# Kernel tuning notes

Hardware: AMD Instinct MI355X
Metric: run time of the kernel (lower is better)

Reference implementation:

```python
import jax, jax.numpy as jnp
import numpy as np

WS = 8          # window size
HEADS = 16      # num heads

def conv2d(x, w, padding=0, groups=1):
    return jax.lax.conv_general_dilated(
        x, w, window_strides=(1, 1),
        padding=((padding, padding), (padding, padding)),
        feature_group_count=groups,
        dimension_numbers=('NCHW', 'OIHW', 'NCHW'))

def bn(x, scale, bias):  # inference BN folded into per-channel affine
    return x * scale[None, :, None, None] + bias[None, :, None, None]

def relative_position_index(ws):
    coords = np.stack(np.meshgrid(np.arange(ws), np.arange(ws), indexing='ij'))  # (2, ws, ws)
    cf = coords.reshape(2, -1)
    rc = (cf[:, :, None] - cf[:, None, :]).transpose(1, 2, 0)  # (n, n, 2)
    rc[:, :, 0] += ws - 1
    rc[:, :, 1] += ws - 1
    rc[:, :, 0] *= 2 * ws - 1
    return rc.sum(-1)  # (n, n) int

def avg_pool(x, kh, kw, ph, pw):
    # AvgPool2d with count_include_pad=True (zero pad, divide by full kernel size)
    s = jax.lax.reduce_window(x, 0.0, jax.lax.add, (1, 1, kh, kw), (1, 1, 1, 1),
                              ((0, 0), (0, 0), (ph, ph), (pw, pw)))
    return s / (kh * kw)

def setup_inputs() -> dict:
    key = jax.random.key(0)
    ks = jax.random.split(key, 12)
    C = 256
    x = jax.random.normal(ks[0], (4, C, 128, 128), dtype=jnp.float32)
    inp = {
        'x': x,
        'qkv_w':     jax.random.normal(ks[1], (3 * C, C, 1, 1), jnp.float32) * 0.05,
        'local1_w':  jax.random.normal(ks[2], (C, C, 3, 3), jnp.float32) * 0.05,
        'local1_scale': jnp.ones((C,), jnp.float32),
        'local1_bias':  jnp.zeros((C,), jnp.float32),
        'local2_w':  jax.random.normal(ks[3], (C, C, 1, 1), jnp.float32) * 0.05,
        'local2_scale': jnp.ones((C,), jnp.float32),
        'local2_bias':  jnp.zeros((C,), jnp.float32),
        'dw_w':      jax.random.normal(ks[4], (C, 1, WS, WS), jnp.float32) * 0.05,
        'proj_scale': jnp.ones((C,), jnp.float32),
        'proj_bias':  jnp.zeros((C,), jnp.float32),
        'pw_w':      jax.random.normal(ks[5], (C, C, 1, 1), jnp.float32) * 0.05,
        'rel_bias_table': jax.random.normal(ks[6], ((2 * WS - 1) ** 2, HEADS), jnp.float32) * 0.02,
    }
    return inp

def reference(x, qkv_w, local1_w, local1_scale, local1_bias,
              local2_w, local2_scale, local2_bias,
              dw_w, proj_scale, proj_bias, pw_w, rel_bias_table):
    B, C, H, W = x.shape
    ws, h = WS, HEADS
    d = C // h
    scale = d ** -0.5

    # local branches
    local = bn(conv2d(x, local2_w, padding=0), local2_scale, local2_bias) \
          + bn(conv2d(x, local1_w, padding=1), local1_scale, local1_bias)

    # reflect-pad to multiple of ws (static shapes)
    pad_h = (ws - H % ws) % ws
    pad_w = (ws - W % ws) % ws
    xp = x
    if pad_w:
        xp = jnp.pad(xp, ((0, 0), (0, 0), (0, 0), (0, pad_w)), mode='reflect')
    if pad_h:
        xp = jnp.pad(xp, ((0, 0), (0, 0), (0, pad_h), (0, 0)), mode='reflect')
    Hp, Wp = xp.shape[2], xp.shape[3]
    hh, ww = Hp // ws, Wp // ws

    # qkv: 1x1 conv, then window partition
    qkv = conv2d(xp, qkv_w)  # (B, 3C, Hp, Wp)
    qkv = qkv.reshape(B, 3, h, d, hh, ws, ww, ws)
    qkv = qkv.transpose(1, 0, 4, 6, 2, 5, 7, 3)  # (3, B, hh, ww, h, ws, ws, d)
    qkv = qkv.reshape(3, B * hh * ww, h, ws * ws, d)
    q, k, v = qkv[0], qkv[1], qkv[2]

    dots = jnp.einsum('whid,whjd->whij', q, k) * scale
    rpi = relative_position_index(ws)  # (n, n)
    bias = rel_bias_table[rpi.reshape(-1)].reshape(ws * ws, ws * ws, h)
    dots = dots + bias.transpose(2, 0, 1)[None]
    attn = jax.nn.softmax(dots, axis=-1)
    out = jnp.einsum('whij,whjd->whid', attn, v)

    # windows back to image
    out = out.reshape(B, hh, ww, h, ws, ws, d)
    out = out.transpose(0, 3, 6, 1, 4, 2, 5).reshape(B, C, Hp, Wp)
    out = out[:, :, :H, :W]

    # boundary smoothing avg pools (reflect pad 1 then zero-padded avg pool)
    ax = avg_pool(jnp.pad(out, ((0, 0), (0, 0), (0, 1), (0, 0)), mode='reflect'),
                  ws, 1, ws // 2 - 1, 0)
    ay = avg_pool(jnp.pad(out, ((0, 0), (0, 0), (0, 0), (0, 1)), mode='reflect'),
                  1, ws, 0, ws // 2 - 1)
    out = ax + ay + local

    # pad_out + separable conv projection
    out = jnp.pad(out, ((0, 0), (0, 0), (0, 1), (0, 1)), mode='reflect')
    out = conv2d(out, dw_w, padding=(ws - 1) // 2, groups=C)  # depthwise 8x8
    out = bn(out, proj_scale, proj_bias)
    out = conv2d(out, pw_w)  # pointwise 1x1
    return out[:, :, :H, :W]
```

## Files before the change

kernel.cpp:

```cpp
#include <hip/hip_runtime.h>
#include <cstddef>

#define HH 128
#define WW2 128
#define HWSZ (HH*WW2)
#define CCH 256

typedef __attribute__((ext_vector_type(8))) short short8v;
typedef __attribute__((ext_vector_type(16))) float f32x16;
typedef __attribute__((ext_vector_type(4)))  float f32x4;

__device__ __forceinline__ ushort bf16rte(float v) {
    uint u = __float_as_uint(v);
    uint r = u + 0x7FFFu + ((u >> 16) & 1u);
    return (ushort)(r >> 16);
}

__global__ __launch_bounds__(256) void k_fold(const float* __restrict__ l1w, const float* __restrict__ l1s,
                                              const float* __restrict__ l1b, const float* __restrict__ l2w,
                                              const float* __restrict__ l2s, const float* __restrict__ l2b,
                                              float* __restrict__ Wf, float* __restrict__ biasf) {
    int idx = blockIdx.x * 256 + threadIdx.x;
    if (idx < 2304 * 256) {
        int co = idx & 255;
        int i2 = idx >> 8;
        int ci = i2 / 9;
        int k  = i2 - ci * 9;
        float w = l1s[co] * l1w[co * 2304 + ci * 9 + k];
        if (k == 4) w += l2s[co] * l2w[co * 256 + ci];
        Wf[i2 * 256 + co] = w;
    }
    if (idx < 256) biasf[idx] = l1b[idx] + l2b[idx];
}

__global__ __launch_bounds__(256) void k_wsplit(const float* __restrict__ Wf,
                                                ushort* __restrict__ ahi, ushort* __restrict__ alo) {
    int idx = blockIdx.x * 256 + threadIdx.x;
    if (idx >= 589824) return;
    int j    = idx & 7;
    int lane = (idx >> 3) & 63;
    int t2   = idx >> 9;
    int kb   = t2 % 144;
    int cob  = t2 / 144;
    int cc  = kb / 18; int rem = kb - cc * 18; int tap = rem >> 1; int ks = rem & 1;
    int ci  = cc * 32 + ks * 16 + ((lane >> 5) << 3) + j;
    int co  = cob * 32 + (lane & 31);
    float v = Wf[(size_t)(ci * 9 + tap) * 256 + co];
    ushort h = bf16rte(v);
    float hf = __uint_as_float((uint)h << 16);
    ushort l = bf16rte(v - hf);
    ahi[idx] = h;
    alo[idx] = l;
}

__global__ __launch_bounds__(256) void k_aswz(const float* __restrict__ qkvw,
                                              ushort* __restrict__ aqh, ushort* __restrict__ aql) {
    int idx = blockIdx.x * 256 + threadIdx.x;
    if (idx >= 196608) return;
    int j    = idx & 7;
    int lane = (idx >> 3) & 63;
    int t2   = idx >> 9;
    int kk   = t2 & 7;
    int hp   = t2 >> 3;
    int p    = hp % 3, h = hp / 3;
    int co = p * 256 + h * 16 + (lane & 15);
    int ci = kk * 32 + ((lane >> 4) << 3) + j;
    float v = qkvw[(size_t)co * 256 + ci];
    ushort hi = bf16rte(v);
    float hf = __uint_as_float((uint)hi << 16);
    aqh[idx] = hi;
    aql[idx] = bf16rte(v - hf);
}

__global__ __launch_bounds__(256) void k_cvt(const float* __restrict__ x,
                                             ushort* __restrict__ xhi, ushort* __restrict__ xlo) {
    __shared__ uint pk[32 * 265];
    int t = threadIdx.x;
    int bid = blockIdx.x;
    int b = bid >> 9;
    int px0 = (bid & 511) * 32;
    const float* xb = x + (size_t)b * CCH * HWSZ;
    for (int step = 0; step < 32; ++step) {
        int ci = step * 8 + (t >> 5);
        float v = xb[(size_t)ci * HWSZ + px0 + (t & 31)];
        ushort h = bf16rte(v);
        float hf = __uint_as_float((uint)h << 16);
        ushort l = bf16rte(v - hf);
        pk[(t & 31) * 265 + ci] = ((uint)h << 16) | l;
    }
    __syncthreads();
    int pxl = t >> 3, o = t & 7;
    uint* hp = (uint*)xhi;
    uint* lp = (uint*)xlo;
    size_t pb2 = ((size_t)b * HWSZ + px0 + pxl) * 128;
#pragma unroll
    for (int m = 0; m < 16; ++m) {
        int cip = m * 16 + o * 2;
        uint p0 = pk[pxl * 265 + cip];
        uint p1 = pk[pxl * 265 + cip + 1];
        hp[pb2 + m * 8 + o] = (p1 & 0xFFFF0000u) | (p0 >> 16);
        lp[pb2 + m * 8 + o] = (p1 << 16) | (p0 & 0xFFFFu);
    }
}

__global__ __launch_bounds__(256) void k_conv3m(const ushort* __restrict__ xhi, const ushort* __restrict__ xlo,
                                                const ushort* __restrict__ afr_hi, const ushort* __restrict__ afr_lo,
                                                const float* __restrict__ biasf, float* __restrict__ outp) {
    __shared__ __align__(16) ushort Xsh[12960];
    char* xsb = (char*)Xsh;

    int t = threadIdx.x;
    int bid = blockIdx.x;
    int cb = bid & 1;
    int t2 = bid >> 1;
    int tile_c = t2 & 7;
    int tile_r = (t2 >> 3) & 15;
    int b = t2 >> 7;
    int x0 = tile_c * 16, y0 = tile_r * 8;

    int w = t >> 6, lane = t & 63;
    int co_w = cb * 128 + (w >> 1) * 64;
    int pr0 = (w & 1) * 4;
    int pr_l = (lane & 31) >> 4;
    int pc = lane & 15;
    int kl = lane >> 5;
    int lb0 = (pr0 + 0 + pr_l) * 1296 + pc * 72 + kl * 16;
    int lb1 = (pr0 + 2 + pr_l) * 1296 + pc * 72 + kl * 16;

    const short8v* Ahi = (const short8v*)afr_hi;
    const short8v* Alo = (const short8v*)afr_lo;
    int cobase = (co_w >> 5) * 144 * 64;

    f32x16 c00 = {}, c01 = {}, c10 = {}, c11 = {};

    for (int cc = 0; cc < 8; ++cc) {
        __syncthreads();
#pragma unroll
        for (int it = 0; it < 6; ++it) {
            int i = t + it * 256;
            if (i < 1440) {
                int oct = i & 3;
                int j2 = i >> 2;
                int plane = j2 & 1;
                int loc = j2 >> 1;
                int r = loc / 18, c = loc - r * 18;
                int gy = y0 - 1 + r, gx = x0 - 1 + c;
                uint4 v = make_uint4(0u, 0u, 0u, 0u);
                if (gy >= 0 && gy < 128 && gx >= 0 && gx < 128) {
                    const ushort* src = plane ? xlo : xhi;
                    v = *(const uint4*)(src + ((size_t)(b * HWSZ + gy * 128 + gx) * 256 + cc * 32 + oct * 8));
                }
                *(uint4*)(xsb + plane * 12960 + loc * 72 + oct * 16) = v;
            }
        }
        __syncthreads();

        int baseA = cobase + cc * 18 * 64 + lane;
#pragma unroll
        for (int tap = 0; tap < 9; ++tap) {
            const int ky = tap / 3, kx = tap - ky * 3;
#pragma unroll
            for (int ks = 0; ks < 2; ++ks) {
                const int boff = ky * 1296 + kx * 72 + ks * 32;
                short8v b0h = *(const short8v*)(xsb + lb0 + boff);
                short8v b0l = *(const short8v*)(xsb + lb0 + boff + 12960);
                short8v b1h = *(const short8v*)(xsb + lb1 + boff);
                short8v b1l = *(const short8v*)(xsb + lb1 + boff + 12960);
                int ai = baseA + (tap * 2 + ks) * 64;
                short8v a0h = Ahi[ai];
                short8v a0l = Alo[ai];
                short8v a1h = Ahi[ai + 144 * 64];
                short8v a1l = Alo[ai + 144 * 64];
                c00 = __builtin_amdgcn_mfma_f32_32x32x16_bf16(a0h, b0h, c00, 0, 0, 0);
                c00 = __builtin_amdgcn_mfma_f32_32x32x16_bf16(a0h, b0l, c00, 0, 0, 0);
                c00 = __builtin_amdgcn_mfma_f32_32x32x16_bf16(a0l, b0h, c00, 0, 0, 0);
                c01 = __builtin_amdgcn_mfma_f32_32x32x16_bf16(a0h, b1h, c01, 0, 0, 0);
                c01 = __builtin_amdgcn_mfma_f32_32x32x16_bf16(a0h, b1l, c01, 0, 0, 0);
                c01 = __builtin_amdgcn_mfma_f32_32x32x16_bf16(a0l, b1h, c01, 0, 0, 0);
                c10 = __builtin_amdgcn_mfma_f32_32x32x16_bf16(a1h, b0h, c10, 0, 0, 0);
                c10 = __builtin_amdgcn_mfma_f32_32x32x16_bf16(a1h, b0l, c10, 0, 0, 0);
                c10 = __builtin_amdgcn_mfma_f32_32x32x16_bf16(a1l, b0h, c10, 0, 0, 0);
                c11 = __builtin_amdgcn_mfma_f32_32x32x16_bf16(a1h, b1h, c11, 0, 0, 0);
                c11 = __builtin_amdgcn_mfma_f32_32x32x16_bf16(a1h, b1l, c11, 0, 0, 0);
                c11 = __builtin_amdgcn_mfma_f32_32x32x16_bf16(a1l, b1h, c11, 0, 0, 0);
            }
        }
    }

    int colg = x0 + pc;
    int row0 = y0 + pr0 + pr_l;
    int row1 = row0 + 2;
#pragma unroll
    for (int r = 0; r < 16; ++r) {
        int rr = (r & 3) + 8 * (r >> 2) + 4 * kl;
        {
            int co = co_w + rr;
            float bv = biasf[co];
            float* ob = outp + ((size_t)(b * CCH + co)) * HWSZ;
            ob[row0 * 128 + colg] = c00[r] + bv;
            ob[row1 * 128 + colg] = c01[r] + bv;
        }
        {
            int co = co_w + 32 + rr;
            float bv = biasf[co];
            float* ob = outp + ((size_t)(b * CCH + co)) * HWSZ;
            ob[row0 * 128 + colg] = c10[r] + bv;
            ob[row1 * 128 + colg] = c11[r] + bv;
        }
    }
}

__global__ __launch_bounds__(256) void k_attn(const ushort* __restrict__ xhi, const ushort* __restrict__ xlo,
                                              const ushort* __restrict__ aqh, const ushort* __restrict__ aql,
                                              const float* __restrict__ bt, float* __restrict__ attnout) {
    extern __shared__ float smem[];
    ushort* Bs  = (ushort*)smem;
    float* qkvb = smem + 16384;

    int t = threadIdx.x;
    int wv = __builtin_amdgcn_readfirstlane(t >> 6);
    int lane = t & 63;
    int widx = blockIdx.x;
    int b = widx >> 8;
    int rem = widx & 255;
    int hy = rem >> 4, wx = rem & 15;
    int y0 = hy * 8, x0 = wx * 8;

#pragma unroll
    for (int it = 0; it < 16; ++it) {
        int i = it * 256 + t;
        int plane = i >> 11;
        int r2 = i & 2047;
        int tok = r2 >> 5, ci8 = r2 & 31;
        int pix = (y0 + (tok >> 3)) * 128 + (x0 + (tok & 7));
        const ushort* src = plane ? xlo : xhi;
        uint4 v = *(const uint4*)(src + ((size_t)b * HWSZ + pix) * 256 + ci8 * 8);
        int lane2 = ((ci8 & 3) << 4) | (tok & 15);
        int fragid = (plane * 4 + (tok >> 4)) * 8 + (ci8 >> 2);
        *(uint4*)(Bs + (size_t)(fragid * 64 + lane2) * 8) = v;
    }
    __syncthreads();

    int irow = wv * 16 + (lane & 15);
    int jg = lane >> 4;
    int iy = irow >> 3, ix = irow & 7;
    int g0 = wv * 3;

    for (int h = 0; h < 16; ++h) {
        f32x4 c0 = {}, c1 = {}, c2 = {};
#pragma unroll
        for (int g = 0; g < 3; ++g) {
            int gid = g0 + g;
            int p = gid >> 2, tt = gid & 3;
            const short8v* Ah = (const short8v*)aqh + (size_t)((h * 3 + p) * 8) * 64 + lane;
            const short8v* Al = (const short8v*)aql + (size_t)((h * 3 + p) * 8) * 64 + lane;
            const short8v* Bh = (const short8v*)Bs + (tt * 8) * 64 + lane;
            const short8v* Bl = (const short8v*)Bs + ((4 + tt) * 8) * 64 + lane;
            f32x4 c = {};
#pragma unroll
            for (int kk = 0; kk < 8; ++kk) {
                short8v ah = Ah[kk * 64], al = Al[kk * 64];
                short8v bh = Bh[kk * 64], bl = Bl[kk * 64];
                c = __builtin_amdgcn_mfma_f32_16x16x32_bf16(ah, bh, c, 0, 0, 0);
                c = __builtin_amdgcn_mfma_f32_16x16x32_bf16(ah, bl, c, 0, 0, 0);
                c = __builtin_amdgcn_mfma_f32_16x16x32_bf16(al, bh, c, 0, 0, 0);
            }
            if (g == 0) c0 = c; else if (g == 1) c1 = c; else c2 = c;
        }
        __syncthreads();
#pragma unroll
        for (int g = 0; g < 3; ++g) {
            int gid = g0 + g;
            int p = gid >> 2, tt = gid & 3;
            int tok = tt * 16 + (lane & 15);
            int row0 = (lane >> 4) * 4;
            f32x4 c = (g == 0) ? c0 : (g == 1) ? c1 : c2;
#pragma unroll
            for (int r = 0; r < 4; ++r)
                qkvb[(p * 16 + row0 + r) * 64 + tok] = c[r];
        }
        __syncthreads();

        float qd[16];
#pragma unroll
        for (int d = 0; d < 16; ++d) qd[d] = qkvb[d * 64 + irow];
        float s[16];
#pragma unroll
        for (int jj = 0; jj < 16; ++jj) s[jj] = 0.f;
#pragma unroll
        for (int d = 0; d < 16; ++d) {
            const float* kp = &qkvb[(16 + d) * 64 + jg * 16];
#pragma unroll
            for (int m = 0; m < 4; ++m) {
                float4 kv = *(const float4*)(kp + m * 4);
                s[m * 4 + 0] += qd[d] * kv.x;
                s[m * 4 + 1] += qd[d] * kv.y;
                s[m * 4 + 2] += qd[d] * kv.z;
                s[m * 4 + 3] += qd[d] * kv.w;
            }
        }
#pragma unroll
        for (int jj = 0; jj < 16; ++jj) {
            int j = jg * 16 + jj;
            int jy = j >> 3, jx = j & 7;
            int rpi = (iy - jy + 7) * 15 + (ix - jx + 7);
            s[jj] = s[jj] * 0.25f + bt[rpi * 16 + h];
        }
        float mx = s[0];
#pragma unroll
        for (int jj = 1; jj < 16; ++jj) mx = fmaxf(mx, s[jj]);
        mx = fmaxf(mx, __shfl_xor(mx, 16));
        mx = fmaxf(mx, __shfl_xor(mx, 32));
        float ls = 0.f;
#pragma unroll
        for (int jj = 0; jj < 16; ++jj) { s[jj] = __expf(s[jj] - mx); ls += s[jj]; }
        ls += __shfl_xor(ls, 16);
        ls += __shfl_xor(ls, 32);
        float inv = 1.0f / ls;
#pragma unroll
        for (int d = 0; d < 16; ++d) {
            const float* vp = &qkvb[(32 + d) * 64 + jg * 16];
            float o0 = 0.f, o1 = 0.f;
#pragma unroll
            for (int m = 0; m < 4; ++m) {
                float4 vvv = *(const float4*)(vp + m * 4);
                o0 += s[m * 4 + 0] * vvv.x + s[m * 4 + 1] * vvv.y;
                o1 += s[m * 4 + 2] * vvv.z + s[m * 4 + 3] * vvv.w;
            }
            float o = o0 + o1;
            o += __shfl_xor(o, 16);
            o += __shfl_xor(o, 32);
            if (jg == 0)
                attnout[((size_t)(b * CCH + h * 16 + d)) * HWSZ + (y0 + iy) * 128 + (x0 + ix)] = o * inv;
        }
    }
}

__global__ __launch_bounds__(256) void k_pools(const float* __restrict__ attnout, const float* __restrict__ localb,
                                               float* __restrict__ sbuf) {
    for (int i = blockIdx.x * 256 + threadIdx.x; i < 4 * CCH * HWSZ; i += gridDim.x * 256) {
        int xc = i & 127;
        int y  = (i >> 7) & 127;
        int bc = i >> 14;
        const float* pl = attnout + (size_t)bc * HWSZ;
        float axs = 0.f;
#pragma unroll
        for (int d = -3; d <= 4; ++d) {
            int t2 = y + d;
            if (t2 >= 0 && t2 < 128) axs += pl[t2 * 128 + xc];
        }
        if (y >= 124) axs += pl[126 * 128 + xc];
        float ays = 0.f;
#pragma unroll
        for (int d = -3; d <= 4; ++d) {
            int t2 = xc + d;
            if (t2 >= 0 && t2 < 128) ays += pl[y * 128 + t2];
        }
        if (xc >= 124) ays += pl[y * 128 + 126];
        sbuf[i] = (axs + ays) * 0.125f + localb[i];
    }
}

__device__ __forceinline__ void dw_loadrow(const float* __restrict__ sp, int trow, int j, float* dst) {
    if (trow < 0 || trow > 128) {
#pragma unroll
        for (int q = 0; q < 8; ++q) dst[q] = 0.f;
        return;
    }
    int sr = (trow == 128) ? 126 : trow;
    const float* rp = sp + sr * 128;
#pragma unroll
    for (int q = 0; q < 8; ++q) {
        int col = j - 3 + q;
        float v = 0.f;
        if (col >= 0 && col <= 128) v = rp[(col == 128) ? 126 : col];
        dst[q] = v;
    }
}

__global__ __launch_bounds__(256) void k_dw(const float* __restrict__ sbuf, const float* __restrict__ dww,
                                            const float* __restrict__ pscale, const float* __restrict__ pbias,
                                            float* __restrict__ tbuf) {
    int t = threadIdx.x;
    int j = t & 127;
    int half = __builtin_amdgcn_readfirstlane(t >> 7);
    int bid = blockIdx.x;
    int c = (bid & 127) * 2 + half;
    int b = bid >> 7;
    const float* sp = sbuf + ((size_t)(b * CCH + c)) * HWSZ;
    float wloc[64];
    const float* dwp = dww + c * 64;
#pragma unroll
    for (int i = 0; i < 64; ++i) wloc[i] = dwp[i];
    float scale = pscale[c], bias = pbias[c];

    float rbuf[8][8];
#pragma unroll
    for (int tr = -3; tr <= 4; ++tr) {
        dw_loadrow(sp, tr, j, rbuf[(tr + 8) & 7]);
    }
    float* op = tbuf + ((size_t)(b * CCH + c)) * HWSZ;
    for (int yb = 0; yb < 16; ++yb) {
#pragma unroll
        for (int k = 0; k < 8; ++k) {
            int y = yb * 8 + k;
            float a0 = 0.f, a1 = 0.f, a2 = 0.f, a3 = 0.f;
#pragma unroll
            for (int p = 0; p < 8; ++p) {
                const int slot = (k + 5 + p) & 7;
                float part = 0.f;
#pragma unroll
                for (int q = 0; q < 8; ++q) part += wloc[p * 8 + q] * rbuf[slot][q];
                if ((p & 3) == 0) a0 += part;
                else if ((p & 3) == 1) a1 += part;
                else if ((p & 3) == 2) a2 += part;
                else a3 += part;
            }
            op[y * 128 + j] = scale * ((a0 + a1) + (a2 + a3)) + bias;
            dw_loadrow(sp, y + 5, j, rbuf[(k + 5) & 7]);
        }
    }
}

__global__ __launch_bounds__(256) void k_pw(const float* __restrict__ tbuf, const float* __restrict__ pww,
                                            float* __restrict__ outp) {
    __shared__ __align__(16) float xs[8][128];
    __shared__ __align__(16) float wsm[8][64];
    int t = threadIdx.x;
    int bid = blockIdx.x;
    int cb = bid & 3;
    int row = bid >> 2;
    int y = row & 127;
    int b = row >> 7;
    int cg = t >> 4;
    int px = (t & 15) * 8;
    float acc[4][8];
#pragma unroll
    for (int c = 0; c < 4; ++c)
#pragma unroll
        for (int j = 0; j < 8; ++j) acc[c][j] = 0.f;
    const float* tb = tbuf + (size_t)b * CCH * HWSZ + y * 128;

    for (int cc = 0; cc < 32; ++cc) {
        __syncthreads();
        {
            int i = t;
#pragma unroll
            for (int it = 0; it < 4; ++it, i += 256) {
                int ci = i >> 7, p = i & 127;
                xs[ci][p] = tb[(size_t)(cc * 8 + ci) * HWSZ + p];
            }
        }
        for (int i = t; i < 512; i += 256) {
            int ci = i >> 6, co = i & 63;
            wsm[ci][co] = pww[(size_t)(cb * 64 + co) * 256 + cc * 8 + ci];
        }
        __syncthreads();
#pragma unroll
        for (int ci = 0; ci < 8; ++ci) {
            float4 w = *(const float4*)&wsm[ci][cg * 4];
            float4 xa = *(const float4*)&xs[ci][px];
            float4 xbv = *(const float4*)&xs[ci][px + 4];
            float xf[8] = {xa.x, xa.y, xa.z, xa.w, xbv.x, xbv.y, xbv.z, xbv.w};
#pragma unroll
            for (int j = 0; j < 8; ++j) {
                acc[0][j] += w.x * xf[j];
                acc[1][j] += w.y * xf[j];
                acc[2][j] += w.z * xf[j];
                acc[3][j] += w.w * xf[j];
            }
        }
    }
#pragma unroll
    for (int c = 0; c < 4; ++c) {
        int co = cb * 64 + cg * 4 + c;
        float* op = outp + ((size_t)(b * CCH + co)) * HWSZ + y * 128 + px;
        *(float4*)op = make_float4(acc[c][0], acc[c][1], acc[c][2], acc[c][3]);
        *(float4*)(op + 4) = make_float4(acc[c][4], acc[c][5], acc[c][6], acc[c][7]);
    }
}

extern "C" void kernel_launch(void* const* d_in, const int* in_sizes, int n_in,
                              void* d_out, int out_size, void* d_ws, size_t ws_size,
                              hipStream_t stream) {
    const float* x    = (const float*)d_in[0];
    const float* qkvw = (const float*)d_in[1];
    const float* l1w  = (const float*)d_in[2];
    const float* l1s  = (const float*)d_in[3];
    const float* l1b  = (const float*)d_in[4];
    const float* l2w  = (const float*)d_in[5];
    const float* l2s  = (const float*)d_in[6];
    const float* l2b  = (const float*)d_in[7];
    const float* dww  = (const float*)d_in[8];
    const float* ps   = (const float*)d_in[9];
    const float* pb   = (const float*)d_in[10];
    const float* pww  = (const float*)d_in[11];
    const float* bt   = (const float*)d_in[12];
    float* out = (float*)d_out;
    float* wsf = (float*)d_ws;

    const size_t nWf = 589824;
    const size_t nPlane = 16777216;
    const size_t nAq = 196608;
    size_t need = (nWf + 256 + 3 * nPlane) * sizeof(float) + (2 * 589824 + 2 * nAq) * sizeof(ushort);
    if (ws_size < need) return;

    float* Wf      = wsf;
    float* biasf   = wsf + nWf;
    float* attnout = wsf + nWf + 256;
    float* localb  = attnout + nPlane;
    float* sbuf    = localb + nPlane;
    float* tbuf    = attnout;
    ushort* xhi = (ushort*)sbuf;
    ushort* xlo = xhi + nPlane;
    ushort* ahi = (ushort*)(sbuf + nPlane);
    ushort* alo = ahi + 589824;
    ushort* aqh = alo + 589824;
    ushort* aql = aqh + nAq;

    const int attn_lds = 65536 + 12288;
    hipFuncSetAttribute((const void*)k_attn, hipFuncAttributeMaxDynamicSharedMemorySize, attn_lds);

    k_fold  <<<2304, 256, 0, stream>>>(l1w, l1s, l1b, l2w, l2s, l2b, Wf, biasf);
    k_wsplit<<<2304, 256, 0, stream>>>(Wf, ahi, alo);
    k_aswz  <<<768,  256, 0, stream>>>(qkvw, aqh, aql);
    k_cvt   <<<2048, 256, 0, stream>>>(x, xhi, xlo);
    k_conv3m<<<1024, 256, 0, stream>>>(xhi, xlo, ahi, alo, biasf, localb);
    k_attn  <<<1024, 256, attn_lds, stream>>>(xhi, xlo, aqh, aql, bt, attnout);
    k_pools <<<4096, 256, 0, stream>>>(attnout, localb, sbuf);
    k_dw    <<<512,  256, 0, stream>>>(sbuf, dww, ps, pb, tbuf);
    k_pw    <<<2048, 256, 0, stream>>>(tbuf, pww, out);
}
```

Measured before the change: 932.9 us.

## Restructure window attention: register-resident X, double-buffered QKV, LDS bias table

The attention kernel no longer stages the window's input tokens in a 64KB LDS buffer. Each wave keeps its 16 tokens' hi/lo bf16 fragments in registers and computes Q/K/V for its own token slice. The per-head QKV projection for head h+1 is computed into a second LDS buffer while head h's softmax and AV run, replacing two barriers per head with one. The relative-position bias table is copied into LDS transposed by head. LDS use drops to roughly 38KB with a launch bound of 3 blocks per CU to raise occupancy, at the cost of higher register pressure and one extra (wrapped) QKV projection for head 0.

Result: faster. 884.2 us (-5.2%).

```diff
diff --git a/kernel.cpp b/kernel.cpp
--- a/kernel.cpp
+++ b/kernel.cpp
@@ -210,12 +210,11 @@
     }
 }
 
-__global__ __launch_bounds__(256) void k_attn(const ushort* __restrict__ xhi, const ushort* __restrict__ xlo,
-                                              const ushort* __restrict__ aqh, const ushort* __restrict__ aql,
-                                              const float* __restrict__ bt, float* __restrict__ attnout) {
-    extern __shared__ float smem[];
-    ushort* Bs  = (ushort*)smem;
-    float* qkvb = smem + 16384;
+__global__ __launch_bounds__(256, 3) void k_attn(const ushort* __restrict__ xhi, const ushort* __restrict__ xlo,
+                                                 const ushort* __restrict__ aqh, const ushort* __restrict__ aql,
+                                                 const float* __restrict__ bt, float* __restrict__ attnout) {
+    __shared__ float qkvb[2][48 * 64];
+    __shared__ float btl[16 * 225];
 
     int t = threadIdx.x;
     int wv = __builtin_amdgcn_readfirstlane(t >> 6);
@@ -226,70 +225,80 @@
     int hy = rem >> 4, wx = rem & 15;
     int y0 = hy * 8, x0 = wx * 8;
 
-#pragma unroll
-    for (int it = 0; it < 16; ++it) {
-        int i = it * 256 + t;
-        int plane = i >> 11;
-        int r2 = i & 2047;
-        int tok = r2 >> 5, ci8 = r2 & 31;
-        int pix = (y0 + (tok >> 3)) * 128 + (x0 + (tok & 7));
-        const ushort* src = plane ? xlo : xhi;
-        uint4 v = *(const uint4*)(src + ((size_t)b * HWSZ + pix) * 256 + ci8 * 8);
-        int lane2 = ((ci8 & 3) << 4) | (tok & 15);
-        int fragid = (plane * 4 + (tok >> 4)) * 8 + (ci8 >> 2);
-        *(uint4*)(Bs + (size_t)(fragid * 64 + lane2) * 8) = v;
+    for (int i = t; i < 3600; i += 256) {
+        int rpi = i >> 4, hh = i & 15;
+        btl[hh * 225 + rpi] = bt[i];
+    }
+
+    int tokb = (wv << 4) | (lane & 15);
+    int pixb = (y0 + (tokb >> 3)) * 128 + (x0 + (tokb & 7));
+    const ushort* xbh = xhi + ((size_t)b * HWSZ + pixb) * 256 + ((lane >> 4) << 3);
+    const ushort* xbl = xlo + ((size_t)b * HWSZ + pixb) * 256 + ((lane >> 4) << 3);
+    short8v bh_[8], bl_[8];
+#pragma unroll
+    for (int kk = 0; kk < 8; ++kk) {
+        bh_[kk] = *(const short8v*)(xbh + kk * 32);
+        bl_[kk] = *(const short8v*)(xbl + kk * 32);
+    }
+
+    const short8v* AhB = (const short8v*)aqh + lane;
+    const short8v* AlB = (const short8v*)aql + lane;
+    int wrow = ((lane >> 4) << 2);
+    int wtok = (wv << 4) + (lane & 15);
+
+    {
+#pragma unroll
+        for (int p = 0; p < 3; ++p) {
+            f32x4 c = {};
+#pragma unroll
+            for (int kk = 0; kk < 8; ++kk) {
+                short8v ah = AhB[(p * 8 + kk) * 64];
+                short8v al = AlB[(p * 8 + kk) * 64];
+                c = __builtin_amdgcn_mfma_f32_16x16x32_bf16(ah, bh_[kk], c, 0, 0, 0);
+                c = __builtin_amdgcn_mfma_f32_16x16x32_bf16(ah, bl_[kk], c, 0, 0, 0);
+                c = __builtin_amdgcn_mfma_f32_16x16x32_bf16(al, bh_[kk], c, 0, 0, 0);
+            }
+            float* bw = &qkvb[0][(p * 16 + wrow) * 64 + wtok];
+            bw[0] = c[0]; bw[64] = c[1]; bw[128] = c[2]; bw[192] = c[3];
+        }
     }
     __syncthreads();
 
     int irow = wv * 16 + (lane & 15);
     int jg = lane >> 4;
     int iy = irow >> 3, ix = irow & 7;
-    int g0 = wv * 3;
-
+
+#pragma unroll 2
     for (int h = 0; h < 16; ++h) {
-        f32x4 c0 = {}, c1 = {}, c2 = {};
-#pragma unroll
-        for (int g = 0; g < 3; ++g) {
-            int gid = g0 + g;
-            int p = gid >> 2, tt = gid & 3;
-            const short8v* Ah = (const short8v*)aqh + (size_t)((h * 3 + p) * 8) * 64 + lane;
-            const short8v* Al = (const short8v*)aql + (size_t)((h * 3 + p) * 8) * 64 + lane;
-            const short8v* Bh = (const short8v*)Bs + (tt * 8) * 64 + lane;
-            const short8v* Bl = (const short8v*)Bs + ((4 + tt) * 8) * 64 + lane;
+        int h2 = (h + 1) & 15;
+        int nb = (h + 1) & 1;
+        const short8v* Ah = AhB + (size_t)h2 * 24 * 64;
+        const short8v* Al = AlB + (size_t)h2 * 24 * 64;
+#pragma unroll
+        for (int p = 0; p < 3; ++p) {
             f32x4 c = {};
 #pragma unroll
             for (int kk = 0; kk < 8; ++kk) {
-                short8v ah = Ah[kk * 64], al = Al[kk * 64];
-                short8v bh = Bh[kk * 64], bl = Bl[kk * 64];
-                c = __builtin_amdgcn_mfma_f32_16x16x32_bf16(ah, bh, c, 0, 0, 0);
-                c = __builtin_amdgcn_mfma_f32_16x16x32_bf16(ah, bl, c, 0, 0, 0);
-                c = __builtin_amdgcn_mfma_f32_16x16x32_bf16(al, bh, c, 0, 0, 0);
-            }
-            if (g == 0) c0 = c; else if (g == 1) c1 = c; else c2 = c;
-        }
-        __syncthreads();
-#pragma unroll
-        for (int g = 0; g < 3; ++g) {
-            int gid = g0 + g;
-            int p = gid >> 2, tt = gid & 3;
-            int tok = tt * 16 + (lane & 15);
-            int row0 = (lane >> 4) * 4;
-            f32x4 c = (g == 0) ? c0 : (g == 1) ? c1 : c2;
-#pragma unroll
-            for (int r = 0; r < 4; ++r)
-                qkvb[(p * 16 + row0 + r) * 64 + tok] = c[r];
-        }
-        __syncthreads();
-
+                short8v ah = Ah[(p * 8 + kk) * 64];
+                short8v al = Al[(p * 8 + kk) * 64];
+                c = __builtin_amdgcn_mfma_f32_16x16x32_bf16(ah, bh_[kk], c, 0, 0, 0);
+                c = __builtin_amdgcn_mfma_f32_16x16x32_bf16(ah, bl_[kk], c, 0, 0, 0);
+                c = __builtin_amdgcn_mfma_f32_16x16x32_bf16(al, bh_[kk], c, 0, 0, 0);
+            }
+            float* bw = &qkvb[nb][(p * 16 + wrow) * 64 + wtok];
+            bw[0] = c[0]; bw[64] = c[1]; bw[128] = c[2]; bw[192] = c[3];
+        }
+
+        const float* buf = qkvb[h & 1];
         float qd[16];
 #pragma unroll
-        for (int d = 0; d < 16; ++d) qd[d] = qkvb[d * 64 + irow];
+        for (int d = 0; d < 16; ++d) qd[d] = buf[d * 64 + irow];
         float s[16];
 #pragma unroll
         for (int jj = 0; jj < 16; ++jj) s[jj] = 0.f;
 #pragma unroll
         for (int d = 0; d < 16; ++d) {
-            const float* kp = &qkvb[(16 + d) * 64 + jg * 16];
+            const float* kp = &buf[(16 + d) * 64 + jg * 16];
 #pragma unroll
             for (int m = 0; m < 4; ++m) {
                 float4 kv = *(const float4*)(kp + m * 4);
@@ -304,7 +313,7 @@
             int j = jg * 16 + jj;
             int jy = j >> 3, jx = j & 7;
             int rpi = (iy - jy + 7) * 15 + (ix - jx + 7);
-            s[jj] = s[jj] * 0.25f + bt[rpi * 16 + h];
+            s[jj] = s[jj] * 0.25f + btl[h * 225 + rpi];
         }
         float mx = s[0];
 #pragma unroll
@@ -319,7 +328,7 @@
         float inv = 1.0f / ls;
 #pragma unroll
         for (int d = 0; d < 16; ++d) {
-            const float* vp = &qkvb[(32 + d) * 64 + jg * 16];
+            const float* vp = &buf[(32 + d) * 64 + jg * 16];
             float o0 = 0.f, o1 = 0.f;
 #pragma unroll
             for (int m = 0; m < 4; ++m) {
@@ -333,6 +342,7 @@
             if (jg == 0)
                 attnout[((size_t)(b * CCH + h * 16 + d)) * HWSZ + (y0 + iy) * 128 + (x0 + ix)] = o * inv;
         }
+        __syncthreads();
     }
 }
 
@@ -518,15 +528,12 @@
     ushort* aqh = alo + 589824;
     ushort* aql = aqh + nAq;
 
-    const int attn_lds = 65536 + 12288;
-    hipFuncSetAttribute((const void*)k_attn, hipFuncAttributeMaxDynamicSharedMemorySize, attn_lds);
-
     k_fold  <<<2304, 256, 0, stream>>>(l1w, l1s, l1b, l2w, l2s, l2b, Wf, biasf);
     k_wsplit<<<2304, 256, 0, stream>>>(Wf, ahi, alo);
     k_aswz  <<<768,  256, 0, stream>>>(qkvw, aqh, aql);
     k_cvt   <<<2048, 256, 0, stream>>>(x, xhi, xlo);
     k_conv3m<<<1024, 256, 0, stream>>>(xhi, xlo, ahi, alo, biasf, localb);
-    k_attn  <<<1024, 256, attn_lds, stream>>>(xhi, xlo, aqh, aql, bt, attnout);
+    k_attn  <<<1024, 256, 0, stream>>>(xhi, xlo, aqh, aql, bt, attnout);
     k_pools <<<4096, 256, 0, stream>>>(attnout, localb, sbuf);
     k_dw    <<<512,  256, 0, stream>>>(sbuf, dww, ps, pb, tbuf);
     k_pw    <<<2048, 256, 0, stream>>>(tbuf, pww, out);
```
